# Kernel optimization log

Hardware: AMD Instinct MI355X
Metric: run time of the kernel (lower is better)

## Reference

```python
import jax, jax.numpy as jnp
import numpy as np

B, S, C_MEL, D_MODEL, K, MAX_DUR = 4, 128, 80, 256, 9, 16
EPS = 1e-5


def setup_inputs():
    key = jax.random.key(0)
    ks = jax.random.split(key, 8)
    rng = np.random.RandomState(0)
    duration = rng.randint(4, MAX_DUR, size=(B, S)).astype(np.int32)
    mel_len = duration.sum(axis=1).astype(np.int32)
    M = int(mel_len.max())
    H = D_MODEL
    def nrm(k, shape, s=0.05):
        return jax.random.normal(k, shape, jnp.float32) * s
    return {
        'mel': jax.random.normal(ks[0], (B, M, C_MEL), jnp.float32),
        'mel_len': jnp.asarray(mel_len),
        'duration': jnp.asarray(duration),
        'src_len': jnp.full((B,), S, dtype=jnp.int32),
        'max_dur': MAX_DUR,
        'conv1_w': nrm(ks[1], (1, K, 1, H), 0.1),
        'bn1_gamma': jnp.ones((H,), jnp.float32),
        'bn1_beta': jnp.zeros((H,), jnp.float32),
        'conv2_w': nrm(ks[2], (1, K, H, 1), 0.05),
        'bn2_gamma': jnp.ones((1,), jnp.float32),
        'bn2_beta': jnp.zeros((1,), jnp.float32),
        'w_ih_f': nrm(ks[3], (3 * H, C_MEL)),
        'w_hh_f': nrm(ks[4], (3 * H, H)),
        'b_ih_f': jnp.zeros((3 * H,), jnp.float32),
        'b_hh_f': jnp.zeros((3 * H,), jnp.float32),
        'w_ih_b': nrm(ks[5], (3 * H, C_MEL)),
        'w_hh_b': nrm(ks[6], (3 * H, H)),
        'b_ih_b': jnp.zeros((3 * H,), jnp.float32),
        'b_hh_b': jnp.zeros((3 * H,), jnp.float32),
    }


def _conv_block(x, w, gamma, beta):
    # x: [N, H=n_mel, W=time, Cin]; conv kernel (1, K) along time, SAME pad, no bias
    p = (w.shape[1] - 1) // 2
    y = jax.lax.conv_general_dilated(x, w, (1, 1), ((0, 0), (p, p)),
                                     dimension_numbers=('NHWC', 'HWIO', 'NHWC'))
    # eval-mode BatchNorm2d (running_mean=0, running_var=1)
    y = y * (gamma / np.sqrt(1.0 + EPS)) + beta
    return jax.nn.relu(y)


def _gru_final(x, mask, w_ih, w_hh, b_ih, b_hh):
    # x: [N, T, C]; mask: [N, T]; returns final hidden state [N, H]
    N, T, _ = x.shape
    H = w_hh.shape[1]
    xg = jnp.einsum('ntc,gc->ntg', x, w_ih) + b_ih  # [N, T, 3H], gates (r,z,n)

    def step(h, inp):
        xg_t, m_t = inp
        hg = h @ w_hh.T + b_hh
        xr, xz, xn = jnp.split(xg_t, 3, axis=-1)
        hr, hz, hn = jnp.split(hg, 3, axis=-1)
        r = jax.nn.sigmoid(xr + hr)
        z = jax.nn.sigmoid(xz + hz)
        n = jnp.tanh(xn + r * hn)
        h_new = (1.0 - z) * n + z * h
        h = jnp.where(m_t[:, None], h_new, h)
        return h, None

    h0 = jnp.zeros((N, H), x.dtype)
    h, _ = jax.lax.scan(step, h0, (xg.swapaxes(0, 1), mask.T))
    return h


def reference(mel, mel_len, duration, src_len, max_dur,
              conv1_w, bn1_gamma, bn1_beta, conv2_w, bn2_gamma, bn2_beta,
              w_ih_f, w_hh_f, b_ih_f, b_hh_f, w_ih_b, w_hh_b, b_ih_b, b_hh_b):
    Bn, M, C = mel.shape
    Sn = duration.shape[1]
    T = max_dur
    t = jnp.arange(T)
    seg_valid = jnp.arange(Sn)[None, :] < src_len[:, None]            # [B, S]
    dur = jnp.where(seg_valid, duration, 0)
    starts = jnp.cumsum(dur, axis=1) - dur                            # [B, S]
    idx = jnp.clip(starts[:, :, None] + t[None, None, :], 0, M - 1)   # [B, S, T]
    mask = t[None, None, :] < dur[:, :, None]                         # [B, S, T]
    segs = jax.vmap(lambda m, i: m[i])(mel, idx.reshape(Bn, -1)).reshape(Bn, Sn, T, C)
    segs = jnp.where(mask[..., None], segs, 0.0)  # zero pad == per-segment conv padding
    N = Bn * Sn
    x = segs.reshape(N, T, C)
    m = mask.reshape(N, T)
    d = dur.reshape(N)
    # conv stack: per mel-channel 1D conv along time, channels 1 -> d_model -> 1
    xc = x.swapaxes(1, 2)[..., None]                                  # [N, C, T, 1]
    xc = _conv_block(xc, conv1_w, bn1_gamma, bn1_beta)                # [N, C, T, D]
    xc = jnp.where(m[:, None, :, None], xc, 0.0)  # restore zero padding between blocks
    xc = _conv_block(xc, conv2_w, bn2_gamma, bn2_beta)                # [N, C, T, 1]
    xg = xc[..., 0].swapaxes(1, 2)                                    # [N, T, C]
    xg = jnp.where(m[..., None], xg, 0.0)
    # bidirectional GRU over each ragged segment; keep only final hidden states
    h_f = _gru_final(xg, m, w_ih_f, w_hh_f, b_ih_f, b_hh_f)
    rev = jnp.clip(d[:, None] - 1 - t[None, :], 0, T - 1)             # reverse within segment
    x_rev = jnp.take_along_axis(xg, rev[..., None], axis=1)
    h_b = _gru_final(x_rev, m, w_ih_b, w_hh_b, b_ih_b, b_hh_b)
    H = w_hh_f.shape[1]
    out = jnp.concatenate([h_f, h_b], axis=-1).reshape(Bn, Sn, 2 * H)
    return jnp.where(seg_valid[..., None], out, 0.0)
```

## Files before the change

### kernel.cpp

```cpp
#include <hip/hip_runtime.h>
#include <hip/hip_bf16.h>
#include <math.h>

#define BB 4
#define SS 128
#define CC 80
#define HH 256
#define KK 9
#define PP 4
#define TT 16
#define NSEG 512
#define G3 768
#define EPSV 1e-5f
#define XKP 96

typedef short bf16x8 __attribute__((ext_vector_type(8)));
typedef float f32x4 __attribute__((ext_vector_type(4)));

#define HSTR 264

__device__ inline ushort f2bf(float f) {
  unsigned x = __float_as_uint(f);
  unsigned r = (x + 0x7FFF + ((x >> 16) & 1)) >> 16;
  return (ushort)r;
}
__device__ inline float fsig(float x) { return 1.f / (1.f + __expf(-x)); }
__device__ inline float ftanh(float x) {
  float e = __expf(2.f * x);
  return 1.f - 2.f / (e + 1.f);
}

__global__ __launch_bounds__(512) void k_prep(const int* __restrict__ duration,
                                              const int* __restrict__ srclen,
                                              int* __restrict__ starts,
                                              int* __restrict__ dur,
                                              int* __restrict__ perm) {
  __shared__ int ds[512];
  __shared__ int hist[17];
  __shared__ int base[17];
  int tid = threadIdx.x;
  int b = tid >> 7, s = tid & 127;
  int v = (s < srclen[b]) ? duration[b * SS + s] : 0;
  ds[tid] = v;
  if (tid < 17) hist[tid] = 0;
  __syncthreads();
  int run = 0;
  for (int s2 = b * 128; s2 < tid; ++s2) run += ds[s2];
  starts[tid] = run;
  dur[tid] = v;
  atomicAdd(&hist[v], 1);
  __syncthreads();
  if (tid == 0) {
    int acc = 0;
    for (int q = 0; q < 17; q++) { base[q] = acc; acc += hist[q]; }
  }
  __syncthreads();
  int rank = atomicAdd(&base[v], 1);
  perm[rank] = tid;
}

__global__ __launch_bounds__(256) void k_wpackc(const float* __restrict__ w1,
                                                const float* __restrict__ g1v,
                                                const float* __restrict__ be1v,
                                                const float* __restrict__ w2,
                                                ushort* __restrict__ wpc) {
  int tid = blockIdx.x * 256 + threadIdx.x;
  if (tid < 8192) {
    int nt = tid >> 9;
    int lane = (tid >> 3) & 63;
    int j = tid & 7;
    int h = nt * 16 + (lane & 15);
    int k = (lane >> 4) * 8 + j;
    float val = 0.f;
    if (k < KK) val = w1[k * HH + h] * (g1v[h] * rsqrtf(1.f + EPSV));
    else if (k == KK) val = be1v[h];
    wpc[tid] = f2bf(val);
  } else if (tid < 12288) {
    int q = tid - 8192;
    int ks = q >> 9;
    int lane = (q >> 3) & 63;
    int j = q & 7;
    int k = lane & 15;
    int h = ks * 32 + (lane >> 4) * 8 + j;
    float val = (k < KK) ? w2[k * HH + h] : 0.f;
    wpc[tid] = f2bf(val);
  }
}

__global__ __launch_bounds__(256) void k_wpackx(const float* __restrict__ wihf,
                                                const float* __restrict__ wihb,
                                                ushort* __restrict__ wpx) {
  int idx = blockIdx.x * 256 + threadIdx.x;
  int j = idx & 7;
  int lane = (idx >> 3) & 63;
  int q = idx >> 9;
  int ks = q % 3;
  int nt = q / 3;
  int n = nt * 16 + (lane & 15);
  int k = ks * 32 + (lane >> 4) * 8 + j;
  float v = 0.f;
  if (k < CC) v = (n < G3) ? wihf[(size_t)n * CC + k]
                           : wihb[(size_t)(n - G3) * CC + k];
  wpx[idx] = f2bf(v);
}

__global__ __launch_bounds__(512, 4) void k_conv(
    const float* __restrict__ mel, const int* __restrict__ starts,
    const int* __restrict__ dur, const ushort* __restrict__ wpc,
    const float* __restrict__ g2v, const float* __restrict__ be2v,
    ushort* __restrict__ xgb, int Mmel) {
  __shared__ __align__(16) ushort xs2[CC][32];
  __shared__ __align__(16) ushort wlc2[4096];
  __shared__ __align__(16) float zs[8][16][18];
  __shared__ __align__(16) float xgs[16][81];

  const int seg = blockIdx.x;
  const int b = seg >> 7;
  const int d = dur[seg];
  const int st = starts[seg];
  const int tid = threadIdx.x;
  const int wv = tid >> 6;
  const int lane = tid & 63;
  const int u = lane & 15;
  const int lgrp = lane >> 4;
  const int hi2 = lgrp >> 1;

  {
    const uint4* src = (const uint4*)(wpc + 8192);
    uint4* dst = (uint4*)wlc2;
    if (tid < 512) dst[tid] = src[tid];
  }
  for (int idx = tid; idx < CC * 16; idx += 512) {
    int c = idx >> 4, t = idx & 15;
    float v = (t < d) ? mel[(size_t)(b * Mmel + st + t) * CC + c] : 0.f;
    xs2[c][t + 4] = f2bf(v);
  }
  for (int idx = tid; idx < CC * 16; idx += 512) {
    int c = idx >> 4, q = idx & 15;
    int p = (q < 4) ? q : (q + 16);
    xs2[c][p] = 0;
  }

  bf16x8 a1r[16];
#pragma unroll
  for (int nt = 0; nt < 16; nt++) {
    a1r[nt] = *(const bf16x8*)&wpc[nt * 512 + lane * 8];
    asm volatile("" : "+v"(a1r[nt]));
  }

  const float g2 = g2v[0] * rsqrtf(1.f + EPSV);
  const float be2 = be2v[0];
  const bool urow = (u < d);
  const unsigned umask = urow ? 0xFFFFFFFFu : 0u;
  const int src0 = (((lane >> 4) & 1) << 5) + u;
  const int src1 = src0 + 16;
  __syncthreads();

#pragma unroll 1
  for (int ci = 0; ci < 10; ci++) {
    const int c = wv * 10 + ci;
    unsigned bw0 = 0, bw1 = 0, bw2 = 0, bw3 = 0;
    if (lgrp == 0) {
      ushort e0 = xs2[c][u + 0], e1 = xs2[c][u + 1];
      ushort e2 = xs2[c][u + 2], e3 = xs2[c][u + 3];
      ushort e4 = xs2[c][u + 4], e5 = xs2[c][u + 5];
      ushort e6 = xs2[c][u + 6], e7 = xs2[c][u + 7];
      bw0 = (unsigned)e0 | ((unsigned)e1 << 16);
      bw1 = (unsigned)e2 | ((unsigned)e3 << 16);
      bw2 = (unsigned)e4 | ((unsigned)e5 << 16);
      bw3 = (unsigned)e6 | ((unsigned)e7 << 16);
    } else if (lgrp == 1) {
      ushort e0 = xs2[c][u + 8];
      bw0 = (unsigned)e0 | (0x3F80u << 16);
    }
    int4 bi4 = make_int4(bw0, bw1, bw2, bw3);
    bf16x8 b1 = *(bf16x8*)&bi4;

    f32x4 accQ = {0.f, 0.f, 0.f, 0.f};

#pragma unroll
    for (int half = 0; half < 2; half++) {
      unsigned P0[8], P1[8];
#pragma unroll
      for (int i = 0; i < 8; i++) {
        f32x4 z = {0.f, 0.f, 0.f, 0.f};
        f32x4 y = __builtin_amdgcn_mfma_f32_16x16x32_bf16(a1r[half * 8 + i],
                                                          b1, z, 0, 0, 0);
        float y0 = fmaxf(y[0], 0.f), y1 = fmaxf(y[1], 0.f);
        float y2 = fmaxf(y[2], 0.f), y3 = fmaxf(y[3], 0.f);
        P0[i] = ((unsigned)__bfloat16_as_ushort(__float2bfloat16(y0)) |
                 ((unsigned)__bfloat16_as_ushort(__float2bfloat16(y1)) << 16)) & umask;
        P1[i] = ((unsigned)__bfloat16_as_ushort(__float2bfloat16(y2)) |
                 ((unsigned)__bfloat16_as_ushort(__float2bfloat16(y3)) << 16)) & umask;
      }
#pragma unroll
      for (int ks2 = 0; ks2 < 4; ks2++) {
        int ks = half * 4 + ks2;
        int v00 = __shfl((int)P0[2 * ks2], src0, 64);
        int v10 = __shfl((int)P0[2 * ks2 + 1], src0, 64);
        unsigned w0 = hi2 ? (unsigned)v10 : (unsigned)v00;
        int v01 = __shfl((int)P1[2 * ks2], src0, 64);
        int v11 = __shfl((int)P1[2 * ks2 + 1], src0, 64);
        unsigned w1 = hi2 ? (unsigned)v11 : (unsigned)v01;
        int v02 = __shfl((int)P0[2 * ks2], src1, 64);
        int v12 = __shfl((int)P0[2 * ks2 + 1], src1, 64);
        unsigned w2 = hi2 ? (unsigned)v12 : (unsigned)v02;
        int v03 = __shfl((int)P1[2 * ks2], src1, 64);
        int v13 = __shfl((int)P1[2 * ks2 + 1], src1, 64);
        unsigned w3 = hi2 ? (unsigned)v13 : (unsigned)v03;
        int4 ai4 = make_int4(w0, w1, w2, w3);
        bf16x8 a2 = *(bf16x8*)&ai4;
        bf16x8 b2 = *(const bf16x8*)&wlc2[ks * 512 + lane * 8];
        accQ = __builtin_amdgcn_mfma_f32_16x16x32_bf16(a2, b2, accQ, 0, 0, 0);
      }
    }

    if (u < KK) {
#pragma unroll
      for (int r = 0; r < 4; r++) zs[wv][lgrp * 4 + r][u] = accQ[r];
    }
    asm volatile("" ::: "memory");

    if (lgrp == 0) {
      float Q = 0.f;
#pragma unroll
      for (int k = 0; k < KK; k++) {
        int idx = u + k - PP;
        if (idx >= 0 && idx < 16) Q += zs[wv][idx][k];
      }
      float qf = urow ? fmaxf(Q * g2 + be2, 0.f) : 0.f;
      xgs[u][c] = qf;
    }
    asm volatile("" ::: "memory");
  }
  __syncthreads();

  for (int idx = tid; idx < 16 * XKP; idx += 512) {
    int t = idx / XKP, kk = idx - t * XKP;
    ushort v = (kk < CC) ? f2bf(xgs[t][kk]) : (ushort)0;
    xgb[(size_t)(seg * TT + t) * XKP + kk] = v;
  }
}

__global__ __launch_bounds__(256) void k_xgate(
    const ushort* __restrict__ xgb, const ushort* __restrict__ wpx,
    const float* __restrict__ bihf, const float* __restrict__ bihb,
    const int* __restrict__ dur, const int* __restrict__ perm,
    float* __restrict__ G) {
  const int tid = threadIdx.x;
  const int w = tid >> 6, lane = tid & 63;
  const int m0 = blockIdx.x * 64 + w * 16;
  const int by = blockIdx.y;
  const int n0 = by * 64;
  const int lrow = lane & 15, lgrp = lane >> 4;
  const int dir = (by < 12) ? 0 : 1;

  const int prank = m0 >> 4;
  const int seg = perm[prank];
  const int d = dur[seg];
  const int t = lrow;
  int ts = dir ? (d - 1 - t) : t;
  ts = min(max(ts, 0), TT - 1);

  bf16x8 a[3];
#pragma unroll
  for (int ks = 0; ks < 3; ks++)
    a[ks] = *(const bf16x8*)&xgb[(size_t)(seg * TT + ts) * XKP + ks * 32 + lgrp * 8];

  const float* bsrc = dir ? bihb : bihf;
  const int nbase = n0 - dir * G3;

#pragma unroll
  for (int ct = 0; ct < 4; ct++) {
    const int nt = by * 4 + ct;
    f32x4 c = {0.f, 0.f, 0.f, 0.f};
#pragma unroll
    for (int ks = 0; ks < 3; ks++) {
      bf16x8 bfrag = *(const bf16x8*)&wpx[(nt * 3 + ks) * 512 + lane * 8];
      c = __builtin_amdgcn_mfma_f32_16x16x32_bf16(a[ks], bfrag, c, 0, 0, 0);
    }
    float bias = bsrc[nbase + ct * 16 + lrow];
#pragma unroll
    for (int r = 0; r < 4; r++)
      G[(size_t)(m0 + lgrp * 4 + r) * 1536 + n0 + ct * 16 + lrow] = c[r] + bias;
  }
}

__global__ __launch_bounds__(256) void k_wpack(const float* __restrict__ whhf,
                                               const float* __restrict__ whhb,
                                               ushort* __restrict__ wp) {
  int tid = blockIdx.x * 256 + threadIdx.x;
  int r = tid;
  int j = r & 7; r >>= 3;
  int lane = r & 63; r >>= 6;
  int ks = r & 7; r >>= 3;
  int tau = r % 6; r /= 6;
  int wv = r & 7; r >>= 3;
  int dir = r;
  int gate = tau >> 1, a = tau & 1;
  int n = gate * 256 + wv * 32 + a * 16 + (lane & 15);
  int k = ks * 32 + (lane >> 4) * 8 + j;
  float v = (dir ? whhb : whhf)[(size_t)n * HH + k];
  wp[tid] = f2bf(v);
}

__global__ __launch_bounds__(512, 2) void k_gru(
    const float* __restrict__ G, const ushort* __restrict__ wp,
    const float* __restrict__ bhhf, const float* __restrict__ bhhb,
    const int* __restrict__ dur, const int* __restrict__ perm,
    float* __restrict__ out) {
  __shared__ short h_lds[2][16 * HSTR];
  __shared__ ushort wlds[8 * 2 * 8 * 512];
  __shared__ int seg_s[16], d_s[16];

  const int tid = threadIdx.x;
  const int bi = blockIdx.x;
  const int dir = bi >> 5;
  const int grp = bi & 31;
  const int wv = tid >> 6;
  const int lane = tid & 63;
  const int lrow = lane & 15;
  const int lgrp = lane >> 4;

  if (tid < 16) {
    int seg = perm[grp * 16 + tid];
    seg_s[tid] = seg;
    d_s[tid] = dur[seg];
  }
  for (int idx = tid; idx < 2 * 16 * HSTR; idx += 512)
    ((short*)h_lds)[idx] = 0;

  const ushort* wb = wp + (size_t)(dir * 8 + wv) * 6 * 8 * 512 + lane * 8;
  bf16x8 wreg[4][8];
#pragma unroll
  for (int tau = 0; tau < 4; tau++)
#pragma unroll
    for (int ks = 0; ks < 8; ks++)
      wreg[tau][ks] = *(const bf16x8*)&wb[(tau * 8 + ks) * 512];
#pragma unroll
  for (int tt2 = 0; tt2 < 2; tt2++)
#pragma unroll
    for (int ks = 0; ks < 8; ks++) {
      bf16x8 v = *(const bf16x8*)&wb[((4 + tt2) * 8 + ks) * 512];
      *(bf16x8*)&wlds[((wv * 2 + tt2) * 8 + ks) * 512 + lane * 8] = v;
    }
  __syncthreads();

  int d4[4], seg4[4];
#pragma unroll
  for (int r = 0; r < 4; r++) {
    d4[r] = d_s[lgrp * 4 + r];
    seg4[r] = seg_s[lgrp * 4 + r];
  }
  int dmax = 0;
#pragma unroll
  for (int q = 0; q < 16; q++) dmax = max(dmax, d_s[q]);

  const int i0 = wv * 32 + lrow;
  const float* bh = dir ? bhhb : bhhf;
  float bias[3][2];
#pragma unroll
  for (int g = 0; g < 3; g++)
#pragma unroll
    for (int a = 0; a < 2; a++) bias[g][a] = bh[g * 256 + i0 + 16 * a];

  size_t gbase[4];
#pragma unroll
  for (int r = 0; r < 4; r++)
    gbase[r] = (size_t)((grp * 16 + lgrp * 4 + r) * 16) * 1536 + dir * G3
               + i0;

  float h[4][2] = {};
  float gxc[4][3][2];
  float gxn[4][3][2];

#pragma unroll
  for (int r = 0; r < 4; r++)
#pragma unroll
    for (int g = 0; g < 3; g++)
#pragma unroll
      for (int a = 0; a < 2; a++)
        gxc[r][g][a] = G[gbase[r] + g * 256 + 16 * a];

  for (int t = 0; t < dmax; t++) {
    const int cur = t & 1;
    const int tn = min(t + 1, TT - 1);
#pragma unroll
    for (int r = 0; r < 4; r++)
#pragma unroll
      for (int g = 0; g < 3; g++)
#pragma unroll
        for (int a = 0; a < 2; a++)
          gxn[r][g][a] = G[gbase[r] + (size_t)tn * 1536 + g * 256 + 16 * a];

    f32x4 acc[6];
#pragma unroll
    for (int tau = 0; tau < 6; tau++) acc[tau] = (f32x4){0.f, 0.f, 0.f, 0.f};
#pragma unroll
    for (int ks = 0; ks < 8; ks++) {
      bf16x8 av = *(const bf16x8*)&h_lds[cur][lrow * HSTR + ks * 32 + lgrp * 8];
#pragma unroll
      for (int tau = 0; tau < 4; tau++)
        acc[tau] = __builtin_amdgcn_mfma_f32_16x16x32_bf16(av, wreg[tau][ks],
                                                           acc[tau], 0, 0, 0);
#pragma unroll
      for (int tt2 = 0; tt2 < 2; tt2++) {
        bf16x8 wf = *(const bf16x8*)&wlds[((wv * 2 + tt2) * 8 + ks) * 512 + lane * 8];
        acc[4 + tt2] = __builtin_amdgcn_mfma_f32_16x16x32_bf16(av, wf,
                                                               acc[4 + tt2], 0, 0, 0);
      }
    }
#pragma unroll
    for (int r = 0; r < 4; r++) {
      if (t < d4[r]) {
#pragma unroll
        for (int a = 0; a < 2; a++) {
          float rr = fsig(gxc[r][0][a] + acc[a][r] + bias[0][a]);
          float zz = fsig(gxc[r][1][a] + acc[2 + a][r] + bias[1][a]);
          float nn = ftanh(gxc[r][2][a] + rr * (acc[4 + a][r] + bias[2][a]));
          h[r][a] = (1.f - zz) * nn + zz * h[r][a];
          h_lds[cur ^ 1][(lgrp * 4 + r) * HSTR + i0 + 16 * a] = (short)f2bf(h[r][a]);
        }
      }
    }
#pragma unroll
    for (int r = 0; r < 4; r++)
#pragma unroll
      for (int g = 0; g < 3; g++)
#pragma unroll
        for (int a = 0; a < 2; a++) gxc[r][g][a] = gxn[r][g][a];
    __syncthreads();
  }

#pragma unroll
  for (int r = 0; r < 4; r++)
#pragma unroll
    for (int a = 0; a < 2; a++)
      out[(size_t)seg4[r] * 512 + dir * 256 + i0 + 16 * a] = h[r][a];
}

extern "C" void kernel_launch(void* const* d_in, const int* in_sizes, int n_in,
                              void* d_out, int out_size, void* d_ws, size_t ws_size,
                              hipStream_t stream) {
  const float* mel = (const float*)d_in[0];
  const int Mmel = in_sizes[0] / (BB * CC);
  const int* duration = (const int*)d_in[2];
  const int* src_len = (const int*)d_in[3];
  const float* conv1_w = (const float*)d_in[5];
  const float* bn1_g = (const float*)d_in[6];
  const float* bn1_b = (const float*)d_in[7];
  const float* conv2_w = (const float*)d_in[8];
  const float* bn2_g = (const float*)d_in[9];
  const float* bn2_b = (const float*)d_in[10];
  const float* w_ih_f = (const float*)d_in[11];
  const float* w_hh_f = (const float*)d_in[12];
  const float* b_ih_f = (const float*)d_in[13];
  const float* b_hh_f = (const float*)d_in[14];
  const float* w_ih_b = (const float*)d_in[15];
  const float* w_hh_b = (const float*)d_in[16];
  const float* b_ih_b = (const float*)d_in[17];
  const float* b_hh_b = (const float*)d_in[18];

  char* w = (char*)d_ws;
  int* starts = (int*)w;            w += 512 * sizeof(int);
  int* dur = (int*)w;               w += 512 * sizeof(int);
  int* perm = (int*)w;              w += 512 * sizeof(int);
  w += 512 * sizeof(int);
  ushort* xgb = (ushort*)w;         w += (size_t)NSEG * TT * XKP * sizeof(ushort);
  float* G = (float*)w;             w += (size_t)NSEG * TT * 1536 * sizeof(float);
  ushort* wp = (ushort*)w;          w += (size_t)2 * 8 * 6 * 8 * 512 * sizeof(ushort);
  ushort* wpc = (ushort*)w;         w += (size_t)12288 * sizeof(ushort);
  ushort* wpx = (ushort*)w;         w += (size_t)96 * 3 * 512 * sizeof(ushort);
  (void)ws_size; (void)n_in; (void)out_size;

  k_prep<<<1, 512, 0, stream>>>(duration, src_len, starts, dur, perm);
  k_wpack<<<1536, 256, 0, stream>>>(w_hh_f, w_hh_b, wp);
  k_wpackc<<<48, 256, 0, stream>>>(conv1_w, bn1_g, bn1_b, conv2_w, wpc);
  k_wpackx<<<576, 256, 0, stream>>>(w_ih_f, w_ih_b, wpx);
  k_conv<<<NSEG, 512, 0, stream>>>(mel, starts, dur, wpc, bn2_g, bn2_b, xgb, Mmel);
  k_xgate<<<dim3(128, 24), 256, 0, stream>>>(xgb, wpx, b_ih_f, b_ih_b, dur, perm, G);
  k_gru<<<64, 512, 0, stream>>>(G, wp, b_hh_f, b_hh_b, dur, perm, (float*)d_out);
}
```

Before: 121.7 us.

## Fuse input-gate GEMM into conv kernel and merge weight-pack kernels

Merges the three weight-packing kernels into one launch. It also folds the input-gate MFMA projection into the tail of the conv kernel, so each segment block computes its own G rows right after producing xgb. An inverse permutation is added in prep so that G rows land in duration-sorted order for the GRU. This cuts two kernel launches and the separate xgb reload, at the cost of more serial per-block work in the conv kernel with only 512 blocks.

```diff
diff --git a/kernel.cpp b/kernel.cpp
--- a/kernel.cpp
+++ b/kernel.cpp
@@ -34,7 +34,8 @@
                                               const int* __restrict__ srclen,
                                               int* __restrict__ starts,
                                               int* __restrict__ dur,
-                                              int* __restrict__ perm) {
+                                              int* __restrict__ perm,
+                                              int* __restrict__ iperm) {
   __shared__ int ds[512];
   __shared__ int hist[17];
   __shared__ int base[17];
@@ -57,58 +58,75 @@
   __syncthreads();
   int rank = atomicAdd(&base[v], 1);
   perm[rank] = tid;
-}
-
-__global__ __launch_bounds__(256) void k_wpackc(const float* __restrict__ w1,
-                                                const float* __restrict__ g1v,
-                                                const float* __restrict__ be1v,
-                                                const float* __restrict__ w2,
-                                                ushort* __restrict__ wpc) {
-  int tid = blockIdx.x * 256 + threadIdx.x;
-  if (tid < 8192) {
-    int nt = tid >> 9;
-    int lane = (tid >> 3) & 63;
-    int j = tid & 7;
-    int h = nt * 16 + (lane & 15);
-    int k = (lane >> 4) * 8 + j;
-    float val = 0.f;
-    if (k < KK) val = w1[k * HH + h] * (g1v[h] * rsqrtf(1.f + EPSV));
-    else if (k == KK) val = be1v[h];
-    wpc[tid] = f2bf(val);
-  } else if (tid < 12288) {
-    int q = tid - 8192;
-    int ks = q >> 9;
+  iperm[tid] = rank;
+}
+
+__global__ __launch_bounds__(256) void k_packall(
+    const float* __restrict__ whhf, const float* __restrict__ whhb,
+    const float* __restrict__ w1, const float* __restrict__ g1v,
+    const float* __restrict__ be1v, const float* __restrict__ w2,
+    const float* __restrict__ wihf, const float* __restrict__ wihb,
+    ushort* __restrict__ wp, ushort* __restrict__ wpc,
+    ushort* __restrict__ wpx) {
+  int idx = blockIdx.x * 256 + threadIdx.x;
+  if (idx < 393216) {
+    int r = idx;
+    int j = r & 7; r >>= 3;
+    int lane = r & 63; r >>= 6;
+    int ks = r & 7; r >>= 3;
+    int tau = r % 6; r /= 6;
+    int wv = r & 7; r >>= 3;
+    int dir = r;
+    int gate = tau >> 1, a = tau & 1;
+    int n = gate * 256 + wv * 32 + a * 16 + (lane & 15);
+    int k = ks * 32 + (lane >> 4) * 8 + j;
+    float v = (dir ? whhb : whhf)[(size_t)n * HH + k];
+    wp[idx] = f2bf(v);
+  } else if (idx < 405504) {
+    int tid = idx - 393216;
+    if (tid < 8192) {
+      int nt = tid >> 9;
+      int lane = (tid >> 3) & 63;
+      int j = tid & 7;
+      int h = nt * 16 + (lane & 15);
+      int k = (lane >> 4) * 8 + j;
+      float val = 0.f;
+      if (k < KK) val = w1[k * HH + h] * (g1v[h] * rsqrtf(1.f + EPSV));
+      else if (k == KK) val = be1v[h];
+      wpc[tid] = f2bf(val);
+    } else {
+      int q = tid - 8192;
+      int ks = q >> 9;
+      int lane = (q >> 3) & 63;
+      int j = q & 7;
+      int k = lane & 15;
+      int h = ks * 32 + (lane >> 4) * 8 + j;
+      float val = (k < KK) ? w2[k * HH + h] : 0.f;
+      wpc[tid] = f2bf(val);
+    }
+  } else {
+    int q = idx - 405504;
+    int j = q & 7;
     int lane = (q >> 3) & 63;
-    int j = q & 7;
-    int k = lane & 15;
-    int h = ks * 32 + (lane >> 4) * 8 + j;
-    float val = (k < KK) ? w2[k * HH + h] : 0.f;
-    wpc[tid] = f2bf(val);
-  }
-}
-
-__global__ __launch_bounds__(256) void k_wpackx(const float* __restrict__ wihf,
-                                                const float* __restrict__ wihb,
-                                                ushort* __restrict__ wpx) {
-  int idx = blockIdx.x * 256 + threadIdx.x;
-  int j = idx & 7;
-  int lane = (idx >> 3) & 63;
-  int q = idx >> 9;
-  int ks = q % 3;
-  int nt = q / 3;
-  int n = nt * 16 + (lane & 15);
-  int k = ks * 32 + (lane >> 4) * 8 + j;
-  float v = 0.f;
-  if (k < CC) v = (n < G3) ? wihf[(size_t)n * CC + k]
-                           : wihb[(size_t)(n - G3) * CC + k];
-  wpx[idx] = f2bf(v);
+    int qq = q >> 9;
+    int ks = qq % 3;
+    int nt = qq / 3;
+    int n = nt * 16 + (lane & 15);
+    int k = ks * 32 + (lane >> 4) * 8 + j;
+    float v = 0.f;
+    if (k < CC) v = (n < G3) ? wihf[(size_t)n * CC + k]
+                             : wihb[(size_t)(n - G3) * CC + k];
+    wpx[q] = f2bf(v);
+  }
 }
 
 __global__ __launch_bounds__(512, 4) void k_conv(
     const float* __restrict__ mel, const int* __restrict__ starts,
-    const int* __restrict__ dur, const ushort* __restrict__ wpc,
+    const int* __restrict__ dur, const int* __restrict__ iperm,
+    const ushort* __restrict__ wpc, const ushort* __restrict__ wpx,
     const float* __restrict__ g2v, const float* __restrict__ be2v,
-    ushort* __restrict__ xgb, int Mmel) {
+    const float* __restrict__ bihf, const float* __restrict__ bihb,
+    ushort* __restrict__ xgb, float* __restrict__ G, int Mmel) {
   __shared__ __align__(16) ushort xs2[CC][32];
   __shared__ __align__(16) ushort wlc2[4096];
   __shared__ __align__(16) float zs[8][16][18];
@@ -240,68 +258,35 @@
     ushort v = (kk < CC) ? f2bf(xgs[t][kk]) : (ushort)0;
     xgb[(size_t)(seg * TT + t) * XKP + kk] = v;
   }
-}
-
-__global__ __launch_bounds__(256) void k_xgate(
-    const ushort* __restrict__ xgb, const ushort* __restrict__ wpx,
-    const float* __restrict__ bihf, const float* __restrict__ bihb,
-    const int* __restrict__ dur, const int* __restrict__ perm,
-    float* __restrict__ G) {
-  const int tid = threadIdx.x;
-  const int w = tid >> 6, lane = tid & 63;
-  const int m0 = blockIdx.x * 64 + w * 16;
-  const int by = blockIdx.y;
-  const int n0 = by * 64;
-  const int lrow = lane & 15, lgrp = lane >> 4;
-  const int dir = (by < 12) ? 0 : 1;
-
-  const int prank = m0 >> 4;
-  const int seg = perm[prank];
-  const int d = dur[seg];
-  const int t = lrow;
-  int ts = dir ? (d - 1 - t) : t;
-  ts = min(max(ts, 0), TT - 1);
-
-  bf16x8 a[3];
-#pragma unroll
-  for (int ks = 0; ks < 3; ks++)
-    a[ks] = *(const bf16x8*)&xgb[(size_t)(seg * TT + ts) * XKP + ks * 32 + lgrp * 8];
-
-  const float* bsrc = dir ? bihb : bihf;
-  const int nbase = n0 - dir * G3;
-
-#pragma unroll
-  for (int ct = 0; ct < 4; ct++) {
-    const int nt = by * 4 + ct;
-    f32x4 c = {0.f, 0.f, 0.f, 0.f};
-#pragma unroll
-    for (int ks = 0; ks < 3; ks++) {
-      bf16x8 bfrag = *(const bf16x8*)&wpx[(nt * 3 + ks) * 512 + lane * 8];
-      c = __builtin_amdgcn_mfma_f32_16x16x32_bf16(a[ks], bfrag, c, 0, 0, 0);
-    }
-    float bias = bsrc[nbase + ct * 16 + lrow];
-#pragma unroll
-    for (int r = 0; r < 4; r++)
-      G[(size_t)(m0 + lgrp * 4 + r) * 1536 + n0 + ct * 16 + lrow] = c[r] + bias;
-  }
-}
-
-__global__ __launch_bounds__(256) void k_wpack(const float* __restrict__ whhf,
-                                               const float* __restrict__ whhb,
-                                               ushort* __restrict__ wp) {
-  int tid = blockIdx.x * 256 + threadIdx.x;
-  int r = tid;
-  int j = r & 7; r >>= 3;
-  int lane = r & 63; r >>= 6;
-  int ks = r & 7; r >>= 3;
-  int tau = r % 6; r /= 6;
-  int wv = r & 7; r >>= 3;
-  int dir = r;
-  int gate = tau >> 1, a = tau & 1;
-  int n = gate * 256 + wv * 32 + a * 16 + (lane & 15);
-  int k = ks * 32 + (lane >> 4) * 8 + j;
-  float v = (dir ? whhb : whhf)[(size_t)n * HH + k];
-  wp[tid] = f2bf(v);
+  __syncthreads();
+
+  {
+    const int prank = iperm[seg];
+    const int dirp = wv >> 2;
+    const int wloc = wv & 3;
+    int ts = dirp ? (d - 1 - u) : u;
+    ts = min(max(ts, 0), TT - 1);
+    bf16x8 a[3];
+#pragma unroll
+    for (int ks = 0; ks < 3; ks++)
+      a[ks] = *(const bf16x8*)&xgb[(size_t)(seg * TT + ts) * XKP + ks * 32 + lgrp * 8];
+    const float* bsrc = dirp ? bihb : bihf;
+#pragma unroll 1
+    for (int ct = 0; ct < 12; ct++) {
+      const int nt = dirp * 48 + wloc * 12 + ct;
+      const int n0g = nt * 16;
+      f32x4 cacc = {0.f, 0.f, 0.f, 0.f};
+#pragma unroll
+      for (int ks = 0; ks < 3; ks++) {
+        bf16x8 bfrag = *(const bf16x8*)&wpx[(nt * 3 + ks) * 512 + lane * 8];
+        cacc = __builtin_amdgcn_mfma_f32_16x16x32_bf16(a[ks], bfrag, cacc, 0, 0, 0);
+      }
+      float bias = bsrc[n0g + u - dirp * G3];
+#pragma unroll
+      for (int r = 0; r < 4; r++)
+        G[(size_t)(prank * 16 + lgrp * 4 + r) * 1536 + n0g + u] = cacc[r] + bias;
+    }
+  }
 }
 
 __global__ __launch_bounds__(512, 2) void k_gru(
@@ -465,7 +450,7 @@
   int* starts = (int*)w;            w += 512 * sizeof(int);
   int* dur = (int*)w;               w += 512 * sizeof(int);
   int* perm = (int*)w;              w += 512 * sizeof(int);
-  w += 512 * sizeof(int);
+  int* iperm = (int*)w;             w += 512 * sizeof(int);
   ushort* xgb = (ushort*)w;         w += (size_t)NSEG * TT * XKP * sizeof(ushort);
   float* G = (float*)w;             w += (size_t)NSEG * TT * 1536 * sizeof(float);
   ushort* wp = (ushort*)w;          w += (size_t)2 * 8 * 6 * 8 * 512 * sizeof(ushort);
@@ -473,11 +458,10 @@
   ushort* wpx = (ushort*)w;         w += (size_t)96 * 3 * 512 * sizeof(ushort);
   (void)ws_size; (void)n_in; (void)out_size;
 
-  k_prep<<<1, 512, 0, stream>>>(duration, src_len, starts, dur, perm);
-  k_wpack<<<1536, 256, 0, stream>>>(w_hh_f, w_hh_b, wp);
-  k_wpackc<<<48, 256, 0, stream>>>(conv1_w, bn1_g, bn1_b, conv2_w, wpc);
-  k_wpackx<<<576, 256, 0, stream>>>(w_ih_f, w_ih_b, wpx);
-  k_conv<<<NSEG, 512, 0, stream>>>(mel, starts, dur, wpc, bn2_g, bn2_b, xgb, Mmel);
-  k_xgate<<<dim3(128, 24), 256, 0, stream>>>(xgb, wpx, b_ih_f, b_ih_b, dur, perm, G);
+  k_prep<<<1, 512, 0, stream>>>(duration, src_len, starts, dur, perm, iperm);
+  k_packall<<<2160, 256, 0, stream>>>(w_hh_f, w_hh_b, conv1_w, bn1_g, bn1_b,
+                                      conv2_w, w_ih_f, w_ih_b, wp, wpc, wpx);
+  k_conv<<<NSEG, 512, 0, stream>>>(mel, starts, dur, iperm, wpc, wpx,
+                                   bn2_g, bn2_b, b_ih_f, b_ih_b, xgb, G, Mmel);
   k_gru<<<64, 512, 0, stream>>>(G, wp, b_hh_f, b_hh_b, dur, perm, (float*)d_out);
 }
```

New measurement: 112.5 us. -7.6%, faster.
